# Kernel tuning notes

Measured on AMD Instinct MI355X. Metric: run time of the kernel, lower is better.

The kernel has to match this reference:

```python
import jax, jax.numpy as jnp
import numpy as np

S, T, B = 48, 32, 64          # src_len, trg_len, batch
H, E, V = 1024, 512, 32000    # hid_dim, emb_dim, vocab
PAD = 1


def setup_inputs() -> dict:
    key = jax.random.key(0)
    ks = jax.random.split(key, 20)
    p = lambda k, shape: jax.random.normal(k, shape, jnp.float32) * 0.02
    z = lambda n: jnp.zeros((n,), jnp.float32)
    return {
        "src": jax.random.randint(ks[0], (S, B), 0, V),
        "trg": jax.random.randint(ks[1], (T, B), 0, V),
        # encoder
        "emb_enc": p(ks[2], (V, E)),
        "Wi_f": p(ks[3], (3 * H, E)), "Wh_f": p(ks[4], (3 * H, H)), "bi_f": z(3 * H), "bh_f": z(3 * H),
        "Wi_b": p(ks[5], (3 * H, E)), "Wh_b": p(ks[6], (3 * H, H)), "bi_b": z(3 * H), "bh_b": z(3 * H),
        "W_fc": p(ks[7], (H, 2 * H)), "b_fc": z(H),
        # attention
        "W_attn": p(ks[8], (H, 3 * H)), "b_attn": z(H), "v_attn": p(ks[9], (H,)),
        # decoder
        "emb_dec": p(ks[10], (V, E)),
        "Wi_d": p(ks[11], (3 * H, 2 * H + E)), "Wh_d": p(ks[12], (3 * H, H)), "bi_d": z(3 * H), "bh_d": z(3 * H),
        "W_out": p(ks[13], (V, 3 * H + E)), "b_out": z(V),
    }


def _gru_step(h, gx, Wh, bh):
    # PyTorch GRU cell: gx = W_i x + b_i (precomputed), gates split [r, z, n]
    gh = h @ Wh.T + bh
    xr, xz, xn = jnp.split(gx, 3, axis=-1)
    hr, hz, hn = jnp.split(gh, 3, axis=-1)
    r = jax.nn.sigmoid(xr + hr)
    zt = jax.nn.sigmoid(xz + hz)
    n = jnp.tanh(xn + r * hn)
    return (1.0 - zt) * n + zt * h


def _run_gru(emb, Wi, Wh, bi, bh):
    gx = jnp.einsum('sbe,ge->sbg', emb, Wi) + bi      # [S,B,3H]
    h0 = jnp.zeros((emb.shape[1], Wh.shape[1]), emb.dtype)
    def step(h, g):
        h2 = _gru_step(h, g, Wh, bh)
        return h2, h2
    hT, outs = jax.lax.scan(step, h0, gx)
    return outs, hT


def reference(src, trg, emb_enc, Wi_f, Wh_f, bi_f, bh_f, Wi_b, Wh_b, bi_b, bh_b,
              W_fc, b_fc, W_attn, b_attn, v_attn, emb_dec, Wi_d, Wh_d, bi_d, bh_d,
              W_out, b_out):
    mask = (src != PAD).T                              # [B,S]
    emb = emb_enc[src]                                 # [S,B,E]
    out_f, hf = _run_gru(emb, Wi_f, Wh_f, bi_f, bh_f)
    out_b_rev, hb = _run_gru(emb[::-1], Wi_b, Wh_b, bi_b, bh_b)
    out_b = out_b_rev[::-1]
    enc_bt = jnp.concatenate([out_f, out_b], -1).transpose(1, 0, 2)  # [B,S,2H]
    hidden = jnp.tanh(jnp.concatenate([hf, hb], -1) @ W_fc.T + b_fc)  # [B,H]

    def attend(h):
        hrep = jnp.broadcast_to(h[:, None, :], (B, S, H))
        energy = jnp.tanh(jnp.concatenate([hrep, enc_bt], -1) @ W_attn.T + b_attn)  # [B,S,H]
        sc = energy @ v_attn                                                        # [B,S]
        sc = jnp.where(mask, sc, jnp.float32(-1e10))
        return jax.nn.softmax(sc, axis=-1)

    def dec_step(h, tok):
        et = emb_dec[tok]                              # [B,E]
        a = attend(h)                                  # [B,S]
        w = jnp.einsum('bs,bsh->bh', a, enc_bt)        # [B,2H]
        gx = jnp.concatenate([et, w], -1) @ Wi_d.T + bi_d
        h2 = _gru_step(h, gx, Wh_d, bh_d)
        pred = jnp.concatenate([h2, w, et], -1) @ W_out.T + b_out  # [B,V]
        return h2, pred

    # teacher_forcing_ratio = 1.0 -> input at step t is trg[t-1]
    _, preds = jax.lax.scan(dec_step, hidden, trg[:-1])           # [T-1,B,V]
    outputs = jnp.concatenate([jnp.zeros((1, B, V), preds.dtype), preds], 0)
    return outputs
```

## Files before the change

### kernel.cpp

```cpp
#include <hip/hip_runtime.h>
#include <hip/hip_bf16.h>


using bf16x8 = __attribute__((ext_vector_type(8))) short;
using f32x4  = __attribute__((ext_vector_type(4))) float;
typedef __hip_bfloat16 bf16;

#define SS 48
#define TT 32
#define BB 64
#define HH 1024
#define EE 512
#define VV 32000

__device__ __forceinline__ short f2bs(float x) {
  return __builtin_bit_cast(short, __float2bfloat16(x));
}

__global__ __launch_bounds__(256) void embed_src(
    const int* __restrict__ src, const float* __restrict__ emb_enc,
    bf16* __restrict__ emb_bf)
{
  int f = blockIdx.x * 256 + threadIdx.x;
  int row = f >> 6;
  int e8 = (f & 63) * 8;
  int tok = src[row];
  const float* p = emb_enc + (size_t)tok * EE + e8;
  float4 a = *(const float4*)p;
  float4 b = *(const float4*)(p + 4);
  bf16x8 v;
  v[0] = f2bs(a.x); v[1] = f2bs(a.y); v[2] = f2bs(a.z); v[3] = f2bs(a.w);
  v[4] = f2bs(b.x); v[5] = f2bs(b.y); v[6] = f2bs(b.z); v[7] = f2bs(b.w);
  *(bf16x8*)((short*)emb_bf + (size_t)row * EE + e8) = v;
}

__global__ __launch_bounds__(256) void gemm_mfma(
    const bf16* __restrict__ A, int lda,
    const float* __restrict__ W, int ldw,
    const float* __restrict__ bias,
    float* __restrict__ C, int ldc,
    int K, int Mstore)
{
  __shared__ __align__(16) short sA[128 * 40];
  __shared__ __align__(16) short sB[128 * 40];
  const int tid = threadIdx.x;
  const int m0 = blockIdx.y * 128;
  const int n0 = blockIdx.x * 128;
  const int lane = tid & 63;
  const int wave = tid >> 6;
  const int wr = wave >> 1, wc = wave & 1;
  const int quad = lane >> 4, l15 = lane & 15;

  f32x4 acc[4][4];
#pragma unroll
  for (int i = 0; i < 4; i++)
#pragma unroll
    for (int j = 0; j < 4; j++) acc[i][j] = f32x4{0.f, 0.f, 0.f, 0.f};

  const short* Ag = (const short*)A;

  for (int k0 = 0; k0 < K; k0 += 32) {
#pragma unroll
    for (int f = 0; f < 2; f++) {
      int idx = tid + f * 256;
      int r = idx >> 2, cg = idx & 3;
      bf16x8 va = *(const bf16x8*)(Ag + (size_t)(m0 + r) * lda + k0 + cg * 8);
      *(bf16x8*)&sA[r * 40 + cg * 8] = va;
      const float* wp = W + (size_t)(n0 + r) * ldw + k0 + cg * 8;
      float4 w0 = *(const float4*)wp;
      float4 w1 = *(const float4*)(wp + 4);
      bf16x8 vb;
      vb[0] = f2bs(w0.x); vb[1] = f2bs(w0.y); vb[2] = f2bs(w0.z); vb[3] = f2bs(w0.w);
      vb[4] = f2bs(w1.x); vb[5] = f2bs(w1.y); vb[6] = f2bs(w1.z); vb[7] = f2bs(w1.w);
      *(bf16x8*)&sB[r * 40 + cg * 8] = vb;
    }
    __syncthreads();
    bf16x8 af[4], bfr[4];
#pragma unroll
    for (int i = 0; i < 4; i++)
      af[i] = *(const bf16x8*)&sA[(wr * 64 + i * 16 + l15) * 40 + quad * 8];
#pragma unroll
    for (int j = 0; j < 4; j++)
      bfr[j] = *(const bf16x8*)&sB[(wc * 64 + j * 16 + l15) * 40 + quad * 8];
#pragma unroll
    for (int i = 0; i < 4; i++)
#pragma unroll
      for (int j = 0; j < 4; j++)
        acc[i][j] = __builtin_amdgcn_mfma_f32_16x16x32_bf16(af[i], bfr[j], acc[i][j], 0, 0, 0);
    __syncthreads();
  }

#pragma unroll
  for (int i = 0; i < 4; i++) {
#pragma unroll
    for (int j = 0; j < 4; j++) {
#pragma unroll
      for (int r = 0; r < 4; r++) {
        int m = m0 + wr * 64 + i * 16 + quad * 4 + r;
        int n = n0 + wc * 64 + j * 16 + l15;
        if (m < Mstore) {
          float v = acc[i][j][r];
          if (bias) v += bias[n];
          C[(size_t)m * ldc + n] = v;
        }
      }
    }
  }
}

__global__ __launch_bounds__(256) void gemm64(
    const float* __restrict__ A, int lda,
    const float* __restrict__ W, int ldw,
    const float* __restrict__ bias,
    float* __restrict__ C, long long csplit, int ldc,
    int M, int Klen)
{
  __shared__ __align__(16) float As[64][20];
  __shared__ __align__(16) float Ws[64][20];
  const int tid = threadIdx.x;
  const int tx = tid & 15, ty = tid >> 4;
  const int n0 = blockIdx.x * 64;
  const int m0 = blockIdx.y * 64;
  const int kbeg = blockIdx.z * Klen;
  float acc[4][4] = {};

  for (int k0 = kbeg; k0 < kbeg + Klen; k0 += 16) {
#pragma unroll
    for (int i = 0; i < 4; i++) {
      int idx = tid + i * 256;
      int r = idx >> 4, c = idx & 15;
      int m = m0 + r;
      As[r][c] = (m < M) ? A[(size_t)m * lda + k0 + c] : 0.f;
      Ws[r][c] = W[(size_t)(n0 + r) * ldw + k0 + c];
    }
    __syncthreads();
#pragma unroll
    for (int kk = 0; kk < 16; kk += 4) {
      float4 a4[4], w4[4];
#pragma unroll
      for (int i = 0; i < 4; i++) a4[i] = *(const float4*)&As[ty + 16 * i][kk];
#pragma unroll
      for (int j = 0; j < 4; j++) w4[j] = *(const float4*)&Ws[tx + 16 * j][kk];
#pragma unroll
      for (int i = 0; i < 4; i++)
#pragma unroll
        for (int j = 0; j < 4; j++) {
          acc[i][j] += a4[i].x * w4[j].x;
          acc[i][j] += a4[i].y * w4[j].y;
          acc[i][j] += a4[i].z * w4[j].z;
          acc[i][j] += a4[i].w * w4[j].w;
        }
    }
    __syncthreads();
  }

  float* Cp = C + (size_t)blockIdx.z * csplit;
#pragma unroll
  for (int i = 0; i < 4; i++) {
    int m = m0 + ty + 16 * i;
    if (m >= M) continue;
#pragma unroll
    for (int j = 0; j < 4; j++) {
      int n = n0 + tx + 16 * j;
      float v = acc[i][j];
      if (bias) v += bias[n];
      Cp[(size_t)m * ldc + n] = v;
    }
  }
}

__device__ __forceinline__ float sigmoidf_(float x) { return 1.f / (1.f + expf(-x)); }

__global__ __launch_bounds__(256) void gru_enc(
    const float* __restrict__ gx_f, const float* __restrict__ gx_b,
    const float* __restrict__ ghf_p, const float* __restrict__ ghb_p,
    const float* __restrict__ bh_f, const float* __restrict__ bh_b,
    float* __restrict__ h_f, float* __restrict__ h_b,
    float* __restrict__ enc, float* __restrict__ hcat, int s)
{
  int idx = blockIdx.x * 256 + threadIdx.x;
  int dir = idx >> 16;
  int r = idx & 65535;
  int b = r >> 10, j = r & 1023;
  const float* gx = dir ? gx_b : gx_f;
  const float* ghp = dir ? ghb_p : ghf_p;
  const float* bh = dir ? bh_b : bh_f;
  float* h = dir ? h_b : h_f;
  int so = dir ? (SS - 1 - s) : s;

  const float* gxr = gx + ((size_t)so * BB + b) * 3072;
  const int base = b * 3072 + j;
  const int P = BB * 3072;
  float hr = ghp[base] + ghp[P + base] + ghp[2 * P + base] + ghp[3 * P + base] + bh[j];
  float hz = ghp[base + 1024] + ghp[P + base + 1024] + ghp[2 * P + base + 1024] + ghp[3 * P + base + 1024] + bh[1024 + j];
  float hn = ghp[base + 2048] + ghp[P + base + 2048] + ghp[2 * P + base + 2048] + ghp[3 * P + base + 2048] + bh[2048 + j];
  float rg = sigmoidf_(gxr[j] + hr);
  float zg = sigmoidf_(gxr[1024 + j] + hz);
  float ng = tanhf(gxr[2048 + j] + rg * hn);
  float hprev = h[b * HH + j];
  float hnew = (1.f - zg) * ng + zg * hprev;
  h[b * HH + j] = hnew;
  enc[((size_t)b * SS + so) * 2048 + dir * 1024 + j] = hnew;
  if (s == SS - 1) hcat[b * 2048 + dir * 1024 + j] = hnew;
}

__global__ __launch_bounds__(256) void combine_hidden(
    const float* __restrict__ hp, const float* __restrict__ b_fc,
    float* __restrict__ h_dec)
{
  int idx = blockIdx.x * 256 + threadIdx.x;
  int j = idx & 1023;
  const int P = BB * HH;
  h_dec[idx] = tanhf(hp[idx] + hp[P + idx] + hp[2 * P + idx] + hp[3 * P + idx] + b_fc[j]);
}

__global__ __launch_bounds__(256) void attn_step(
    const float* __restrict__ dpp,
    const float* __restrict__ enc_proj,
    const float* __restrict__ v_attn,
    const float* __restrict__ enc,
    const int* __restrict__ src,
    const int* __restrict__ trg,
    const float* __restrict__ emb_dec,
    int t,
    float* __restrict__ dec_in,
    bf16* __restrict__ feat)
{
  __shared__ float dp[1024];
  __shared__ float sc[SS];
  __shared__ float aw[SS];
  const int b = blockIdx.x;
  const int tid = threadIdx.x;
  const int P = BB * HH;
  for (int j = tid; j < 1024; j += 256)
    dp[j] = dpp[b * HH + j] + dpp[P + b * HH + j] + dpp[2 * P + b * HH + j] + dpp[3 * P + b * HH + j];
  __syncthreads();

  const int lane = tid & 63, w = tid >> 6;
  for (int s = w; s < SS; s += 4) {
    float p = 0.f;
    const float* ep = enc_proj + ((size_t)b * SS + s) * HH;
    for (int j = lane; j < 1024; j += 64)
      p += tanhf(dp[j] + ep[j]) * v_attn[j];
#pragma unroll
    for (int off = 32; off; off >>= 1) p += __shfl_down(p, off);
    if (lane == 0) sc[s] = p;
  }
  __syncthreads();

  if (tid < 64) {
    float v = -3.0e38f;
    if (tid < SS) v = (src[tid * BB + b] != 1) ? sc[tid] : -1.0e10f;
    float mx = v;
#pragma unroll
    for (int off = 32; off; off >>= 1) mx = fmaxf(mx, __shfl_xor(mx, off));
    float e = (tid < SS) ? expf(v - mx) : 0.f;
    float sum = e;
#pragma unroll
    for (int off = 32; off; off >>= 1) sum += __shfl_xor(sum, off);
    if (tid < SS) aw[tid] = e / sum;
  }
  __syncthreads();

  bf16* frow = feat + ((size_t)t * BB + b) * 3584;
  for (int k = tid; k < 2048; k += 256) {
    float acc = 0.f;
    const float* er = enc + ((size_t)b * SS) * 2048 + k;
#pragma unroll 4
    for (int s = 0; s < SS; s++) acc += aw[s] * er[(size_t)s * 2048];
    dec_in[b * 2560 + 512 + k] = acc;
    frow[1024 + k] = __float2bfloat16(acc);
  }
  const int tok = trg[t * BB + b];
  for (int e = tid; e < 512; e += 256) {
    float ev = emb_dec[(size_t)tok * EE + e];
    dec_in[b * 2560 + e] = ev;
    frow[3072 + e] = __float2bfloat16(ev);
  }
}

__global__ __launch_bounds__(256) void gru_dec(
    const float* __restrict__ gxp, const float* __restrict__ ghp,
    const float* __restrict__ bi, const float* __restrict__ bh,
    float* __restrict__ h, bf16* __restrict__ feat, int t)
{
  int idx = blockIdx.x * 256 + threadIdx.x;
  int b = idx >> 10, j = idx & 1023;
  const int base = b * 3072 + j;
  const int P = BB * 3072;
  float xr = gxp[base] + gxp[P + base] + gxp[2 * P + base] + gxp[3 * P + base] + bi[j];
  float xz = gxp[base + 1024] + gxp[P + base + 1024] + gxp[2 * P + base + 1024] + gxp[3 * P + base + 1024] + bi[1024 + j];
  float xn = gxp[base + 2048] + gxp[P + base + 2048] + gxp[2 * P + base + 2048] + gxp[3 * P + base + 2048] + bi[2048 + j];
  float hr = ghp[base] + ghp[P + base] + ghp[2 * P + base] + ghp[3 * P + base] + bh[j];
  float hz = ghp[base + 1024] + ghp[P + base + 1024] + ghp[2 * P + base + 1024] + ghp[3 * P + base + 1024] + bh[1024 + j];
  float hn = ghp[base + 2048] + ghp[P + base + 2048] + ghp[2 * P + base + 2048] + ghp[3 * P + base + 2048] + bh[2048 + j];
  float rg = sigmoidf_(xr + hr);
  float zg = sigmoidf_(xz + hz);
  float ng = tanhf(xn + rg * hn);
  float hprev = h[idx];
  float hnew = (1.f - zg) * ng + zg * hprev;
  h[idx] = hnew;
  feat[((size_t)t * BB + b) * 3584 + j] = __float2bfloat16(hnew);
}

extern "C" void kernel_launch(void* const* d_in, const int* in_sizes, int n_in,
                              void* d_out, int out_size, void* d_ws, size_t ws_size,
                              hipStream_t stream)
{
  const int* src = (const int*)d_in[0];
  const int* trg = (const int*)d_in[1];
  const float* emb_enc = (const float*)d_in[2];
  const float* Wi_f = (const float*)d_in[3];
  const float* Wh_f = (const float*)d_in[4];
  const float* bi_f = (const float*)d_in[5];
  const float* bh_f = (const float*)d_in[6];
  const float* Wi_b = (const float*)d_in[7];
  const float* Wh_b = (const float*)d_in[8];
  const float* bi_b = (const float*)d_in[9];
  const float* bh_b = (const float*)d_in[10];
  const float* W_fc = (const float*)d_in[11];
  const float* b_fc = (const float*)d_in[12];
  const float* W_attn = (const float*)d_in[13];
  const float* b_attn = (const float*)d_in[14];
  const float* v_attn = (const float*)d_in[15];
  const float* emb_dec = (const float*)d_in[16];
  const float* Wi_d = (const float*)d_in[17];
  const float* Wh_d = (const float*)d_in[18];
  const float* bi_d = (const float*)d_in[19];
  const float* bh_d = (const float*)d_in[20];
  const float* W_out = (const float*)d_in[21];
  const float* b_out = (const float*)d_in[22];
  float* out = (float*)d_out;

  size_t off = 0;
  auto alloc = [&](size_t bytes) {
    void* r = (char*)d_ws + off;
    off += (bytes + 255) & ~(size_t)255;
    return r;
  };
  bf16* emb_bf   = (bf16*)alloc((size_t)SS * BB * EE * 2);
  float* gx_f    = (float*)alloc((size_t)SS * BB * 3072 * 4);
  float* gx_b    = (float*)alloc((size_t)SS * BB * 3072 * 4);
  float* ghf_p   = (float*)alloc((size_t)4 * BB * 3072 * 4);
  float* ghb_p   = (float*)alloc((size_t)4 * BB * 3072 * 4);
  float* h_f     = (float*)alloc((size_t)BB * HH * 4);
  float* h_b     = (float*)alloc((size_t)BB * HH * 4);
  float* enc     = (float*)alloc((size_t)BB * SS * 2048 * 4);
  float* hcat    = (float*)alloc((size_t)BB * 2048 * 4);
  float* hp      = (float*)alloc((size_t)4 * BB * HH * 4);
  float* h_dec   = (float*)alloc((size_t)BB * HH * 4);
  float* enc_proj= (float*)alloc((size_t)BB * SS * HH * 4);
  float* dpp     = (float*)alloc((size_t)4 * BB * HH * 4);
  float* dec_in  = (float*)alloc((size_t)BB * 2560 * 4);
  float* gxdp    = (float*)alloc((size_t)4 * BB * 3072 * 4);
  float* ghdp    = (float*)alloc((size_t)4 * BB * 3072 * 4);
  bf16* feat     = (bf16*)alloc((size_t)2048 * 3584 * 2);

  hipMemsetAsync(h_f, 0, (size_t)BB * HH * 4, stream);
  hipMemsetAsync(h_b, 0, (size_t)BB * HH * 4, stream);
  hipMemsetAsync(d_out, 0, (size_t)BB * VV * 4, stream);

  embed_src<<<768, 256, 0, stream>>>(src, emb_enc, emb_bf);
  gemm_mfma<<<dim3(24, 24), 256, 0, stream>>>(emb_bf, 512, Wi_f, 512, bi_f, gx_f, 3072, 512, 3072);
  gemm_mfma<<<dim3(24, 24), 256, 0, stream>>>(emb_bf, 512, Wi_b, 512, bi_b, gx_b, 3072, 512, 3072);

  for (int s = 0; s < SS; s++) {
    gemm64<<<dim3(48, 1, 4), 256, 0, stream>>>(h_f, 1024, Wh_f, 1024, nullptr, ghf_p, (long long)BB * 3072, 3072, 64, 256);
    gemm64<<<dim3(48, 1, 4), 256, 0, stream>>>(h_b, 1024, Wh_b, 1024, nullptr, ghb_p, (long long)BB * 3072, 3072, 64, 256);
    gru_enc<<<512, 256, 0, stream>>>(gx_f, gx_b, ghf_p, ghb_p, bh_f, bh_b, h_f, h_b, enc, hcat, s);
  }

  gemm64<<<dim3(16, 1, 4), 256, 0, stream>>>(hcat, 2048, W_fc, 2048, nullptr, hp, (long long)BB * HH, 1024, 64, 512);
  combine_hidden<<<256, 256, 0, stream>>>(hp, b_fc, h_dec);

  gemm64<<<dim3(16, 48, 1), 256, 0, stream>>>(enc, 2048, W_attn + 1024, 3072, b_attn, enc_proj, 0, 1024, 3072, 2048);

  for (int t = 0; t < TT - 1; t++) {
    gemm64<<<dim3(16, 1, 4), 256, 0, stream>>>(h_dec, 1024, W_attn, 3072, nullptr, dpp, (long long)BB * HH, 1024, 64, 256);
    attn_step<<<64, 256, 0, stream>>>(dpp, enc_proj, v_attn, enc, src, trg, emb_dec, t, dec_in, feat);
    gemm64<<<dim3(48, 1, 4), 256, 0, stream>>>(dec_in, 2560, Wi_d, 2560, nullptr, gxdp, (long long)BB * 3072, 3072, 64, 640);
    gemm64<<<dim3(48, 1, 4), 256, 0, stream>>>(h_dec, 1024, Wh_d, 1024, nullptr, ghdp, (long long)BB * 3072, 3072, 64, 256);
    gru_dec<<<256, 256, 0, stream>>>(gxdp, ghdp, bi_d, bh_d, h_dec, feat, t);
  }

  gemm_mfma<<<dim3(250, 16), 256, 0, stream>>>(feat, 3584, W_out, 3584, b_out,
                                               out + (size_t)BB * VV, VV, 3584, 1984);
}
```

Baseline: 13.33 ms.

## Fuse encoder GRU recurrence into persistent kernel and merge decoder hidden GEMMs

```diff
diff --git a/kernel.cpp b/kernel.cpp
--- a/kernel.cpp
+++ b/kernel.cpp
@@ -12,10 +12,12 @@
 #define HH 1024
 #define EE 512
 #define VV 32000
+#define NBLK_E 256
 
 __device__ __forceinline__ short f2bs(float x) {
   return __builtin_bit_cast(short, __float2bfloat16(x));
 }
+__device__ __forceinline__ float sigmoidf_(float x) { return 1.f / (1.f + expf(-x)); }
 
 __global__ __launch_bounds__(256) void embed_src(
     const int* __restrict__ src, const float* __restrict__ emb_enc,
@@ -44,8 +46,8 @@
   __shared__ __align__(16) short sA[128 * 40];
   __shared__ __align__(16) short sB[128 * 40];
   const int tid = threadIdx.x;
-  const int m0 = blockIdx.y * 128;
-  const int n0 = blockIdx.x * 128;
+  const int m0 = blockIdx.x * 128;
+  const int n0 = blockIdx.y * 128;
   const int lane = tid & 63;
   const int wave = tid >> 6;
   const int wr = wave >> 1, wc = wave & 1;
@@ -169,39 +171,85 @@
   }
 }
 
-__device__ __forceinline__ float sigmoidf_(float x) { return 1.f / (1.f + expf(-x)); }
-
-__global__ __launch_bounds__(256) void gru_enc(
+__device__ __forceinline__ void gbar(int* bar, int target) {
+  __syncthreads();
+  if (threadIdx.x == 0) {
+    __threadfence();
+    __hip_atomic_fetch_add(bar, 1, __ATOMIC_RELAXED, __HIP_MEMORY_SCOPE_AGENT);
+    while (__hip_atomic_load(bar, __ATOMIC_RELAXED, __HIP_MEMORY_SCOPE_AGENT) < target)
+      __builtin_amdgcn_s_sleep(2);
+    __threadfence();
+  }
+  __syncthreads();
+}
+
+__global__ __launch_bounds__(512) void enc_gru_persistent(
     const float* __restrict__ gx_f, const float* __restrict__ gx_b,
-    const float* __restrict__ ghf_p, const float* __restrict__ ghb_p,
+    const float* __restrict__ Wh_f, const float* __restrict__ Wh_b,
     const float* __restrict__ bh_f, const float* __restrict__ bh_b,
-    float* __restrict__ h_f, float* __restrict__ h_b,
-    float* __restrict__ enc, float* __restrict__ hcat, int s)
-{
-  int idx = blockIdx.x * 256 + threadIdx.x;
-  int dir = idx >> 16;
-  int r = idx & 65535;
-  int b = r >> 10, j = r & 1023;
+    float* __restrict__ ht,
+    float* __restrict__ enc,
+    float* __restrict__ hcat,
+    int* __restrict__ bar)
+{
+  __shared__ float gh_l[3][8][64];
+  const int tid = threadIdx.x;
+  const int bid = blockIdx.x;
+  const int dir = bid >> 7;
+  const int j0 = (bid & 127) * 8;
   const float* gx = dir ? gx_b : gx_f;
-  const float* ghp = dir ? ghb_p : ghf_p;
+  const float* Wh = dir ? Wh_b : Wh_f;
   const float* bh = dir ? bh_b : bh_f;
-  float* h = dir ? h_b : h_f;
-  int so = dir ? (SS - 1 - s) : s;
-
-  const float* gxr = gx + ((size_t)so * BB + b) * 3072;
-  const int base = b * 3072 + j;
-  const int P = BB * 3072;
-  float hr = ghp[base] + ghp[P + base] + ghp[2 * P + base] + ghp[3 * P + base] + bh[j];
-  float hz = ghp[base + 1024] + ghp[P + base + 1024] + ghp[2 * P + base + 1024] + ghp[3 * P + base + 1024] + bh[1024 + j];
-  float hn = ghp[base + 2048] + ghp[P + base + 2048] + ghp[2 * P + base + 2048] + ghp[3 * P + base + 2048] + bh[2048 + j];
-  float rg = sigmoidf_(gxr[j] + hr);
-  float zg = sigmoidf_(gxr[1024 + j] + hz);
-  float ng = tanhf(gxr[2048 + j] + rg * hn);
-  float hprev = h[b * HH + j];
-  float hnew = (1.f - zg) * ng + zg * hprev;
-  h[b * HH + j] = hnew;
-  enc[((size_t)b * SS + so) * 2048 + dir * 1024 + j] = hnew;
-  if (s == SS - 1) hcat[b * 2048 + dir * 1024 + j] = hnew;
+  const int lane = tid & 63;
+  const int wv = __builtin_amdgcn_readfirstlane(tid >> 6);
+  const int j = j0 + wv;
+  const float* w0 = Wh + (size_t)j * 1024;
+  const float* w1 = Wh + (size_t)(1024 + j) * 1024;
+  const float* w2 = Wh + (size_t)(2048 + j) * 1024;
+
+  const int b2 = tid & 63, jl2 = tid >> 6;
+  const int jj2 = j0 + jl2;
+  const float bh0 = bh[jj2], bh1 = bh[1024 + jj2], bh2 = bh[2048 + jj2];
+
+  for (int s = 0; s < SS; s++) {
+    const int cur = s & 1;
+    float a0 = 0.f, a1 = 0.f, a2 = 0.f;
+    if (s) {
+      const float* hb = ht + ((size_t)(cur * 2 + dir) * 1024) * 64 + lane;
+#pragma unroll 2
+      for (int k = 0; k < 1024; k += 8) {
+        float hv[8];
+#pragma unroll
+        for (int i = 0; i < 8; i++) hv[i] = hb[(size_t)(k + i) * 64];
+#pragma unroll
+        for (int i = 0; i < 8; i++) {
+          a0 = fmaf(w0[k + i], hv[i], a0);
+          a1 = fmaf(w1[k + i], hv[i], a1);
+          a2 = fmaf(w2[k + i], hv[i], a2);
+        }
+      }
+    }
+    gh_l[0][wv][lane] = a0;
+    gh_l[1][wv][lane] = a1;
+    gh_l[2][wv][lane] = a2;
+    __syncthreads();
+
+    const int so = dir ? (SS - 1 - s) : s;
+    const float* gxr = gx + ((size_t)so * BB + b2) * 3072 + jj2;
+    float hr = gh_l[0][jl2][b2] + bh0;
+    float hz = gh_l[1][jl2][b2] + bh1;
+    float hn = gh_l[2][jl2][b2] + bh2;
+    float rg = sigmoidf_(gxr[0] + hr);
+    float zg = sigmoidf_(gxr[1024] + hz);
+    float ng = tanhf(gxr[2048] + rg * hn);
+    float hprev = ht[((size_t)(cur * 2 + dir) * 1024 + jj2) * 64 + b2];
+    float hnew = (1.f - zg) * ng + zg * hprev;
+    ht[((size_t)((cur ^ 1) * 2 + dir) * 1024 + jj2) * 64 + b2] = hnew;
+    enc[((size_t)b2 * SS + so) * 2048 + dir * 1024 + jj2] = hnew;
+    if (s == SS - 1) hcat[b2 * 2048 + dir * 1024 + jj2] = hnew;
+
+    if (s + 1 < SS) gbar(bar, (s + 1) * NBLK_E);
+  }
 }
 
 __global__ __launch_bounds__(256) void combine_hidden(
@@ -214,8 +262,20 @@
   h_dec[idx] = tanhf(hp[idx] + hp[P + idx] + hp[2 * P + idx] + hp[3 * P + idx] + b_fc[j]);
 }
 
+__global__ __launch_bounds__(256) void build_wdh(
+    const float* __restrict__ Wh_d, const float* __restrict__ W_attn,
+    float* __restrict__ Wcat)
+{
+  int i = blockIdx.x * 256 + threadIdx.x;
+  int r = i >> 8, c4 = (i & 255) * 4;
+  float4 v;
+  if (r < 3072) v = *(const float4*)(Wh_d + (size_t)r * 1024 + c4);
+  else          v = *(const float4*)(W_attn + (size_t)(r - 3072) * 3072 + c4);
+  *(float4*)(Wcat + (size_t)r * 1024 + c4) = v;
+}
+
 __global__ __launch_bounds__(256) void attn_step(
-    const float* __restrict__ dpp,
+    const float* __restrict__ ghdpc,
     const float* __restrict__ enc_proj,
     const float* __restrict__ v_attn,
     const float* __restrict__ enc,
@@ -231,17 +291,19 @@
   __shared__ float aw[SS];
   const int b = blockIdx.x;
   const int tid = threadIdx.x;
-  const int P = BB * HH;
-  for (int j = tid; j < 1024; j += 256)
-    dp[j] = dpp[b * HH + j] + dpp[P + b * HH + j] + dpp[2 * P + b * HH + j] + dpp[3 * P + b * HH + j];
+  const int PG = BB * 4096;
+  for (int jj = tid; jj < 1024; jj += 256) {
+    int base = b * 4096 + 3072 + jj;
+    dp[jj] = ghdpc[base] + ghdpc[PG + base] + ghdpc[2 * PG + base] + ghdpc[3 * PG + base];
+  }
   __syncthreads();
 
   const int lane = tid & 63, w = tid >> 6;
   for (int s = w; s < SS; s += 4) {
     float p = 0.f;
     const float* ep = enc_proj + ((size_t)b * SS + s) * HH;
-    for (int j = lane; j < 1024; j += 64)
-      p += tanhf(dp[j] + ep[j]) * v_attn[j];
+    for (int jj = lane; jj < 1024; jj += 64)
+      p += tanhf(dp[jj] + ep[jj]) * v_attn[jj];
 #pragma unroll
     for (int off = 32; off; off >>= 1) p += __shfl_down(p, off);
     if (lane == 0) sc[s] = p;
@@ -286,14 +348,16 @@
 {
   int idx = blockIdx.x * 256 + threadIdx.x;
   int b = idx >> 10, j = idx & 1023;
-  const int base = b * 3072 + j;
-  const int P = BB * 3072;
-  float xr = gxp[base] + gxp[P + base] + gxp[2 * P + base] + gxp[3 * P + base] + bi[j];
-  float xz = gxp[base + 1024] + gxp[P + base + 1024] + gxp[2 * P + base + 1024] + gxp[3 * P + base + 1024] + bi[1024 + j];
-  float xn = gxp[base + 2048] + gxp[P + base + 2048] + gxp[2 * P + base + 2048] + gxp[3 * P + base + 2048] + bi[2048 + j];
-  float hr = ghp[base] + ghp[P + base] + ghp[2 * P + base] + ghp[3 * P + base] + bh[j];
-  float hz = ghp[base + 1024] + ghp[P + base + 1024] + ghp[2 * P + base + 1024] + ghp[3 * P + base + 1024] + bh[1024 + j];
-  float hn = ghp[base + 2048] + ghp[P + base + 2048] + ghp[2 * P + base + 2048] + ghp[3 * P + base + 2048] + bh[2048 + j];
+  const int xb = b * 3072 + j;
+  const int PX = BB * 3072;
+  const int gb = b * 4096 + j;
+  const int PG = BB * 4096;
+  float xr = gxp[xb] + gxp[PX + xb] + gxp[2 * PX + xb] + gxp[3 * PX + xb] + bi[j];
+  float xz = gxp[xb + 1024] + gxp[PX + xb + 1024] + gxp[2 * PX + xb + 1024] + gxp[3 * PX + xb + 1024] + bi[1024 + j];
+  float xn = gxp[xb + 2048] + gxp[PX + xb + 2048] + gxp[2 * PX + xb + 2048] + gxp[3 * PX + xb + 2048] + bi[2048 + j];
+  float hr = ghp[gb] + ghp[PG + gb] + ghp[2 * PG + gb] + ghp[3 * PG + gb] + bh[j];
+  float hz = ghp[gb + 1024] + ghp[PG + gb + 1024] + ghp[2 * PG + gb + 1024] + ghp[3 * PG + gb + 1024] + bh[1024 + j];
+  float hn = ghp[gb + 2048] + ghp[PG + gb + 2048] + ghp[2 * PG + gb + 2048] + ghp[3 * PG + gb + 2048] + bh[2048 + j];
   float rg = sigmoidf_(xr + hr);
   float zg = sigmoidf_(xz + hz);
   float ng = tanhf(xn + rg * hn);
@@ -341,34 +405,30 @@
   bf16* emb_bf   = (bf16*)alloc((size_t)SS * BB * EE * 2);
   float* gx_f    = (float*)alloc((size_t)SS * BB * 3072 * 4);
   float* gx_b    = (float*)alloc((size_t)SS * BB * 3072 * 4);
-  float* ghf_p   = (float*)alloc((size_t)4 * BB * 3072 * 4);
-  float* ghb_p   = (float*)alloc((size_t)4 * BB * 3072 * 4);
-  float* h_f     = (float*)alloc((size_t)BB * HH * 4);
-  float* h_b     = (float*)alloc((size_t)BB * HH * 4);
+  float* ht      = (float*)alloc((size_t)2 * 2 * 1024 * 64 * 4);
   float* enc     = (float*)alloc((size_t)BB * SS * 2048 * 4);
   float* hcat    = (float*)alloc((size_t)BB * 2048 * 4);
   float* hp      = (float*)alloc((size_t)4 * BB * HH * 4);
   float* h_dec   = (float*)alloc((size_t)BB * HH * 4);
   float* enc_proj= (float*)alloc((size_t)BB * SS * HH * 4);
-  float* dpp     = (float*)alloc((size_t)4 * BB * HH * 4);
   float* dec_in  = (float*)alloc((size_t)BB * 2560 * 4);
   float* gxdp    = (float*)alloc((size_t)4 * BB * 3072 * 4);
-  float* ghdp    = (float*)alloc((size_t)4 * BB * 3072 * 4);
+  float* ghdpc   = (float*)alloc((size_t)4 * BB * 4096 * 4);
+  float* Wdh_cat = (float*)alloc((size_t)4096 * 1024 * 4);
   bf16* feat     = (bf16*)alloc((size_t)2048 * 3584 * 2);
-
-  hipMemsetAsync(h_f, 0, (size_t)BB * HH * 4, stream);
-  hipMemsetAsync(h_b, 0, (size_t)BB * HH * 4, stream);
+  int* bar       = (int*)alloc(256);
+
+  hipMemsetAsync(ht, 0, (size_t)2 * 1024 * 64 * 4, stream);
+  hipMemsetAsync(bar, 0, 256, stream);
   hipMemsetAsync(d_out, 0, (size_t)BB * VV * 4, stream);
 
   embed_src<<<768, 256, 0, stream>>>(src, emb_enc, emb_bf);
   gemm_mfma<<<dim3(24, 24), 256, 0, stream>>>(emb_bf, 512, Wi_f, 512, bi_f, gx_f, 3072, 512, 3072);
   gemm_mfma<<<dim3(24, 24), 256, 0, stream>>>(emb_bf, 512, Wi_b, 512, bi_b, gx_b, 3072, 512, 3072);
-
-  for (int s = 0; s < SS; s++) {
-    gemm64<<<dim3(48, 1, 4), 256, 0, stream>>>(h_f, 1024, Wh_f, 1024, nullptr, ghf_p, (long long)BB * 3072, 3072, 64, 256);
-    gemm64<<<dim3(48, 1, 4), 256, 0, stream>>>(h_b, 1024, Wh_b, 1024, nullptr, ghb_p, (long long)BB * 3072, 3072, 64, 256);
-    gru_enc<<<512, 256, 0, stream>>>(gx_f, gx_b, ghf_p, ghb_p, bh_f, bh_b, h_f, h_b, enc, hcat, s);
-  }
+  build_wdh<<<4096, 256, 0, stream>>>(Wh_d, W_attn, Wdh_cat);
+
+  enc_gru_persistent<<<NBLK_E, 512, 0, stream>>>(gx_f, gx_b, Wh_f, Wh_b, bh_f, bh_b,
+                                                 ht, enc, hcat, bar);
 
   gemm64<<<dim3(16, 1, 4), 256, 0, stream>>>(hcat, 2048, W_fc, 2048, nullptr, hp, (long long)BB * HH, 1024, 64, 512);
   combine_hidden<<<256, 256, 0, stream>>>(hp, b_fc, h_dec);
@@ -376,13 +436,12 @@
   gemm64<<<dim3(16, 48, 1), 256, 0, stream>>>(enc, 2048, W_attn + 1024, 3072, b_attn, enc_proj, 0, 1024, 3072, 2048);
 
   for (int t = 0; t < TT - 1; t++) {
-    gemm64<<<dim3(16, 1, 4), 256, 0, stream>>>(h_dec, 1024, W_attn, 3072, nullptr, dpp, (long long)BB * HH, 1024, 64, 256);
-    attn_step<<<64, 256, 0, stream>>>(dpp, enc_proj, v_attn, enc, src, trg, emb_dec, t, dec_in, feat);
+    gemm64<<<dim3(64, 1, 4), 256, 0, stream>>>(h_dec, 1024, Wdh_cat, 1024, nullptr, ghdpc, (long long)BB * 4096, 4096, 64, 256);
+    attn_step<<<64, 256, 0, stream>>>(ghdpc, enc_proj, v_attn, enc, src, trg, emb_dec, t, dec_in, feat);
     gemm64<<<dim3(48, 1, 4), 256, 0, stream>>>(dec_in, 2560, Wi_d, 2560, nullptr, gxdp, (long long)BB * 3072, 3072, 64, 640);
-    gemm64<<<dim3(48, 1, 4), 256, 0, stream>>>(h_dec, 1024, Wh_d, 1024, nullptr, ghdp, (long long)BB * 3072, 3072, 64, 256);
-    gru_dec<<<256, 256, 0, stream>>>(gxdp, ghdp, bi_d, bh_d, h_dec, feat, t);
-  }
-
-  gemm_mfma<<<dim3(250, 16), 256, 0, stream>>>(feat, 3584, W_out, 3584, b_out,
+    gru_dec<<<256, 256, 0, stream>>>(gxdp, ghdpc, bi_d, bh_d, h_dec, feat, t);
+  }
+
+  gemm_mfma<<<dim3(16, 250), 256, 0, stream>>>(feat, 3584, W_out, 3584, b_out,
                                                out + (size_t)BB * VV, VV, 3584, 1984);
 }
```

Result: faster. 12.85 ms (-3.6%).
